# Kernel tuning notes

Hardware: AMD Instinct MI355X
Metric: run time of the kernel (lower is better)

Reference implementation:

```python
import jax, jax.numpy as jnp
import numpy as np

HEADS = 8
DIM_HEAD = 64
EPS = 1e-5

def setup_inputs() -> dict:
    key = jax.random.key(0)
    ks = jax.random.split(key, 5)
    c, inner = 320, HEADS * DIM_HEAD
    s = 0.02
    return {
        "hidden_states": jax.random.normal(ks[0], (4, c, 16, 32, 32), jnp.float32),
        "ln_w": jnp.ones((c,), jnp.float32),
        "ln_b": jnp.zeros((c,), jnp.float32),
        "Wq": jax.random.normal(ks[1], (inner, c), jnp.float32) * s,
        "Wk": jax.random.normal(ks[2], (inner, c), jnp.float32) * s,
        "Wv": jax.random.normal(ks[3], (inner, c), jnp.float32) * s,
        "Wo": jax.random.normal(ks[4], (c, inner), jnp.float32) * s,
        "bo": jnp.zeros((c,), jnp.float32),
    }

def reference(hidden_states, ln_w, ln_b, Wq, Wk, Wv, Wo, bo):
    b, c, t, h, w = hidden_states.shape
    scale = DIM_HEAD ** (-0.5)
    # (b h w) t c
    x0 = jnp.transpose(hidden_states, (0, 3, 4, 2, 1)).reshape(b * h * w, t, c)
    # LayerNorm over channel dim
    mu = jnp.mean(x0, axis=-1, keepdims=True)
    var = jnp.var(x0, axis=-1, keepdims=True)
    xn = (x0 - mu) / jnp.sqrt(var + EPS) * ln_w + ln_b
    # QKV projections (self-attention: encoder_hidden_states = normed hidden)
    q = xn @ Wq.T  # [B, t, inner]
    k = xn @ Wk.T
    v = xn @ Wv.T
    B = b * h * w
    q = q.reshape(B, t, HEADS, DIM_HEAD)
    k = k.reshape(B, t, HEADS, DIM_HEAD)
    v = v.reshape(B, t, HEADS, DIM_HEAD)
    scores = jnp.einsum("bqhd,bkhd->bhqk", q, k) * scale
    probs = jax.nn.softmax(scores, axis=-1)
    out = jnp.einsum("bhqk,bkhd->bqhd", probs, v).reshape(B, t, HEADS * DIM_HEAD)
    out = out @ Wo.T + bo
    out = out + x0  # residual (dropout p=0)
    # back to b c t h w
    return jnp.transpose(out.reshape(b, h, w, t, c), (0, 4, 3, 1, 2))
```

## Files before the change

kernel.cpp:

```cpp
#include <hip/hip_runtime.h>

#define TT 16
#define CC 320
#define NHEADS 8
#define DH 64
#define INNER 512

typedef float f32x4 __attribute__((ext_vector_type(4)));
typedef float f32x16 __attribute__((ext_vector_type(16)));
typedef short bf16x8 __attribute__((ext_vector_type(8)));
typedef unsigned short u16;

#define Z16 {0.f,0.f,0.f,0.f,0.f,0.f,0.f,0.f,0.f,0.f,0.f,0.f,0.f,0.f,0.f,0.f}

__device__ __forceinline__ float bf2f(u16 u){
    union { unsigned int i; float f; } v; v.i = ((unsigned int)u) << 16; return v.f;
}
__device__ __forceinline__ u16 f2bf(float f){
    union { float f; unsigned int i; } v; v.f = f;
    unsigned int x = v.i;
    return (u16)((x + 0x7fffu + ((x >> 16) & 1u)) >> 16);
}

__global__ __launch_bounds__(256) void k_wprep(const float* __restrict__ wq, const float* __restrict__ wk,
                                               const float* __restrict__ wv, const float* __restrict__ wo,
                                               u16* __restrict__ dqkv, u16* __restrict__ dwo){
    int blk = blockIdx.x;
    if (blk < 240){
        int gid  = blk * 256 + threadIdx.x;
        int lane = gid & 63;
        int f    = gid >> 6;
        int local = f % 12;
        int kl   = local & 1;
        int nblk = local >> 1;
        int c    = (f / 12) % 10;
        int hd   = f / 120;
        int kk   = c * 2 + kl;
        const float* W = (nblk < 2) ? wq : (nblk < 4) ? wk : wv;
        int n  = hd * DH + (nblk & 1) * 32 + (lane & 31);
        int k0 = kk * 16 + (lane >> 5) * 8;
        const float* src = W + (size_t)n * CC + k0;
        f32x4 v0 = *(const f32x4*)src;
        f32x4 v1 = *(const f32x4*)(src + 4);
        bf16x8 o;
        o[0] = (short)f2bf(v0[0]); o[1] = (short)f2bf(v0[1]);
        o[2] = (short)f2bf(v0[2]); o[3] = (short)f2bf(v0[3]);
        o[4] = (short)f2bf(v1[0]); o[5] = (short)f2bf(v1[1]);
        o[6] = (short)f2bf(v1[2]); o[7] = (short)f2bf(v1[3]);
        *(bf16x8*)(dqkv + (size_t)gid * 8) = o;
    } else {
        int gid  = (blk - 240) * 256 + threadIdx.x;
        int lane = gid & 63;
        int f    = gid >> 6;
        int kt   = f & 31;
        int nb   = f >> 5;
        int n  = nb * 32 + (lane & 31);
        int k0 = kt * 16 + (lane >> 5) * 8;
        const float* src = wo + (size_t)n * INNER + k0;
        f32x4 v0 = *(const f32x4*)src;
        f32x4 v1 = *(const f32x4*)(src + 4);
        bf16x8 o;
        o[0] = (short)f2bf(v0[0]); o[1] = (short)f2bf(v0[1]);
        o[2] = (short)f2bf(v0[2]); o[3] = (short)f2bf(v0[3]);
        o[4] = (short)f2bf(v1[0]); o[5] = (short)f2bf(v1[1]);
        o[6] = (short)f2bf(v1[2]); o[7] = (short)f2bf(v1[3]);
        *(bf16x8*)(dwo + (size_t)gid * 8) = o;
    }
}

__global__ __launch_bounds__(256) void k_ln(const float* __restrict__ x, const float* __restrict__ lnw,
                                            const float* __restrict__ lnb, u16* __restrict__ xnf){
    __shared__ float tile[CC][37];
    __shared__ float psum[32][36];
    __shared__ float psq[32][36];
    __shared__ float meanb[32];
    __shared__ float rstdb[32];
    __shared__ float lnw_s[CC];
    __shared__ float lnb_s[CC];

    int wg = blockIdx.x;
    int t = wg & 15, h = (wg >> 4) & 31, b = wg >> 9;
    int tid = threadIdx.x;
    const size_t base = ((size_t)(b * CC) * TT + t) * 1024 + h * 32;

    if (tid < CC - 256){ lnw_s[256 + tid] = lnw[256 + tid]; lnb_s[256 + tid] = lnb[256 + tid]; }
    lnw_s[tid] = lnw[tid]; lnb_s[tid] = lnb[tid];

    int w4 = (tid & 7) * 4, cg = tid >> 3;
    f32x4 s4 = {0.f,0.f,0.f,0.f}, q4 = {0.f,0.f,0.f,0.f};
    for (int i = 0; i < 10; ++i){
        int c = cg * 10 + i;
        f32x4 v = *(const f32x4*)(x + base + (size_t)c * 16384 + w4);
        tile[c][w4 + 0] = v[0]; tile[c][w4 + 1] = v[1];
        tile[c][w4 + 2] = v[2]; tile[c][w4 + 3] = v[3];
        s4 += v; q4 += v * v;
    }
    psum[cg][w4 + 0] = s4[0]; psum[cg][w4 + 1] = s4[1]; psum[cg][w4 + 2] = s4[2]; psum[cg][w4 + 3] = s4[3];
    psq [cg][w4 + 0] = q4[0]; psq [cg][w4 + 1] = q4[1]; psq [cg][w4 + 2] = q4[2]; psq [cg][w4 + 3] = q4[3];
    __syncthreads();

    if (tid < 32){
        float s = 0.f, q = 0.f;
        for (int g = 0; g < 32; ++g){ s += psum[g][tid]; q += psq[g][tid]; }
        float mean = s * (1.f / CC);
        float var  = q * (1.f / CC) - mean * mean;
        meanb[tid] = mean;
        rstdb[tid] = rsqrtf(var + 1e-5f);
    }
    __syncthreads();

    int s_base = (b * 32 + h) * 32;
    #pragma unroll
    for (int j = 0; j < 5; ++j){
        int u = tid + 256 * j;
        int w = u / 40, c8 = u % 40;
        float mean = meanb[w], rstd = rstdb[w];
        int s = s_base + w;
        int row = ((s & 1) << 4) | t;
        int kk = c8 >> 1;
        int lane_f = ((c8 & 1) << 5) | row;
        size_t m32 = (size_t)(s >> 1);
        bf16x8 o;
        #pragma unroll
        for (int e = 0; e < 8; ++e){
            int c = c8 * 8 + e;
            float nv = (tile[c][w] - mean) * rstd * lnw_s[c] + lnb_s[c];
            o[e] = (short)f2bf(nv);
        }
        *(bf16x8*)(xnf + ((size_t)(m32 * 20 + kk) * 64 + lane_f) * 8) = o;
    }
}

#define QH(w,s,r,c) smem[((((w)*2+(s))*16+(r))*72) + (c)]
#define KH(w,s,r,c) smem[9216 + ((((w)*2+(s))*16+(r))*72) + (c)]
#define VT(w,s,d,k) smem[18432 + ((((w)*2+(s))*64+(d))*36) + (k)]

__global__ __launch_bounds__(256, 2) void k_attn(const u16* __restrict__ xnf,
                                                 const u16* __restrict__ wqkv,
                                                 u16* __restrict__ aot){
    __shared__ u16 smem[36864];

    const int tid  = threadIdx.x;
    const int lane = tid & 63;
    const int wid  = tid >> 6;
    const int l31  = lane & 31;
    const int h32  = lane >> 5;
    const int l15  = lane & 15;
    const int g4   = lane >> 4;
    const int m32  = blockIdx.x * 4 + wid;
    const f32x4 zero4 = {0.f, 0.f, 0.f, 0.f};

    #pragma unroll
    for (int j = 0; j < 32; ++j){
        int idx = j * 64 + lane;
        int smp = idx >> 10;
        int d   = (idx >> 4) & 63;
        VT(wid, smp, d, 16 + (idx & 15)) = 0;
    }

    bf16x8 a_f[20];
    {
        const u16* xp = xnf + ((size_t)m32 * 20 * 64 + lane) * 8;
        #pragma unroll
        for (int kk = 0; kk < 20; ++kk)
            a_f[kk] = *(const bf16x8*)(xp + kk * 512);
    }

    #define STAGE(hd_, c_) do {                                                        \
        const u16* gsrc_ = wqkv + ((size_t)((hd_) * 10 + (c_)) * 6144);                \
        u16* ldst_ = (u16*)smem + ((c_) % 3) * 6144;                                   \
        _Pragma("unroll")                                                              \
        for (int i_ = 0; i_ < 3; ++i_)                                                 \
            __builtin_amdgcn_global_load_lds(                                          \
                (const __attribute__((address_space(1))) void*)(gsrc_ + (tid + i_ * 256) * 8), \
                (__attribute__((address_space(3))) void*)(ldst_ + (tid + i_ * 256) * 8),       \
                16, 0, 0);                                                             \
    } while (0)

    for (int hd = 0; hd < NHEADS; ++hd){
        __builtin_amdgcn_sched_barrier(0);
        __builtin_amdgcn_s_barrier();
        __builtin_amdgcn_sched_barrier(0);

        STAGE(hd, 0);

        f32x16 acc[6];
        #pragma unroll
        for (int nb = 0; nb < 6; ++nb) acc[nb] = (f32x16)Z16;

        #pragma unroll
        for (int c = 0; c < 10; ++c){
            asm volatile("s_waitcnt vmcnt(0)" ::: "memory");
            __builtin_amdgcn_sched_barrier(0);
            __builtin_amdgcn_s_barrier();
            __builtin_amdgcn_sched_barrier(0);
            if (c < 9) STAGE(hd, c + 1);
            const u16* wb = (const u16*)smem + (c % 3) * 6144;
            #pragma unroll
            for (int kl = 0; kl < 2; ++kl){
                #pragma unroll
                for (int nb = 0; nb < 6; ++nb){
                    bf16x8 b = *(const bf16x8*)(wb + (nb * 2 + kl) * 512 + lane * 8);
                    acc[nb] = __builtin_amdgcn_mfma_f32_32x32x16_bf16(a_f[c * 2 + kl], b, acc[nb], 0, 0, 0);
                }
            }
            __builtin_amdgcn_sched_barrier(0);
        }
        __builtin_amdgcn_s_barrier();
        __builtin_amdgcn_sched_barrier(0);

        #pragma unroll
        for (int r = 0; r < 16; ++r){
            int row = (r & 3) + 8 * (r >> 2) + 4 * h32;
            int smp = row >> 4, tr = row & 15;
            QH(wid, smp, tr, l31)      = f2bf(acc[0][r] * 0.125f);
            QH(wid, smp, tr, 32 + l31) = f2bf(acc[1][r] * 0.125f);
            KH(wid, smp, tr, l31)      = f2bf(acc[2][r]);
            KH(wid, smp, tr, 32 + l31) = f2bf(acc[3][r]);
            VT(wid, smp, l31, tr)      = f2bf(acc[4][r]);
            VT(wid, smp, 32 + l31, tr) = f2bf(acc[5][r]);
        }

        #pragma unroll
        for (int smp = 0; smp < 2; ++smp){
            f32x4 sc = zero4;
            #pragma unroll
            for (int k0 = 0; k0 < DH; k0 += 32){
                bf16x8 qa = *(const bf16x8*)&QH(wid, smp, l15, k0 + g4 * 8);
                bf16x8 kb = *(const bf16x8*)&KH(wid, smp, l15, k0 + g4 * 8);
                sc = __builtin_amdgcn_mfma_f32_16x16x32_bf16(qa, kb, sc, 0, 0, 0);
            }
            f32x4 pr;
            #pragma unroll
            for (int r = 0; r < 4; ++r){
                float m = sc[r];
                m = fmaxf(m, __shfl_xor(m, 1)); m = fmaxf(m, __shfl_xor(m, 2));
                m = fmaxf(m, __shfl_xor(m, 4)); m = fmaxf(m, __shfl_xor(m, 8));
                float e = __expf(sc[r] - m);
                float ss = e;
                ss += __shfl_xor(ss, 1); ss += __shfl_xor(ss, 2);
                ss += __shfl_xor(ss, 4); ss += __shfl_xor(ss, 8);
                pr[r] = e / ss;
            }
            #pragma unroll
            for (int r = 0; r < 4; ++r){
                QH(wid, smp, g4 * 4 + r, l15) = f2bf(pr[r]);
                QH(wid, smp, g4 * 4 + r, 16 + l15) = 0;
            }
            bf16x8 pa = *(const bf16x8*)&QH(wid, smp, l15, g4 * 8);
            #pragma unroll
            for (int nb = 0; nb < 4; ++nb){
                bf16x8 vb = *(const bf16x8*)&VT(wid, smp, nb * 16 + l15, g4 * 8);
                f32x4 at = __builtin_amdgcn_mfma_f32_16x16x32_bf16(pa, vb, zero4, 0, 0, 0);
                #pragma unroll
                for (int r = 0; r < 4; ++r)
                    KH(wid, smp, g4 * 4 + r, nb * 16 + l15) = f2bf(at[r]);
            }
            const size_t sg = (size_t)m32 * 2 + smp;
            #pragma unroll
            for (int kkl = 0; kkl < 2; ++kkl){
                bf16x8 o8 = *(const bf16x8*)&KH(wid, smp, l15, kkl * 32 + g4 * 8);
                *(bf16x8*)(aot + ((size_t)l15 * 4096 + sg) * 512 + hd * 64 + kkl * 32 + g4 * 8) = o8;
            }
        }
    }
    #undef STAGE
}

__global__ __launch_bounds__(256) void k_oproj_res(const u16* __restrict__ aot, const u16* __restrict__ wof,
                                                   const float* __restrict__ bo, const float* __restrict__ x,
                                                   float* __restrict__ out){
    __shared__ u16 atile[32 * 516];
    __shared__ float otile[4][32 * 36];

    const int tid  = threadIdx.x;
    const int lane = tid & 63;
    const int wid  = tid >> 6;
    const int l31  = lane & 31;
    const int h32  = lane >> 5;
    int wg = blockIdx.x;
    int t = wg & 15, h = (wg >> 4) & 31, b = wg >> 9;
    const int s0 = (b * 32 + h) * 32;

    {
        const u16* src = aot + ((size_t)t * 4096 + s0) * 512;
        #pragma unroll
        for (int i = 0; i < 8; ++i){
            int flat = tid + 256 * i;
            int row = flat >> 6, c16 = flat & 63;
            bf16x8 v = *(const bf16x8*)(src + (size_t)flat * 8);
            *(bf16x8*)(atile + row * 516 + c16 * 8) = v;
        }
    }
    __syncthreads();

    const int nb_start = (wid < 2) ? wid * 3 : 6 + (wid - 2) * 2;
    const int nb_count = (wid < 2) ? 3 : 2;

    for (int j = 0; j < nb_count; ++j){
        const int nb = nb_start + j;
        f32x16 acc = (f32x16)Z16;
        const u16* wp = wof + ((size_t)(nb * 32) * 64 + lane) * 8;
        #pragma unroll
        for (int kt = 0; kt < 32; ++kt){
            bf16x8 af = *(const bf16x8*)(atile + l31 * 516 + kt * 16 + h32 * 8);
            bf16x8 bf = *(const bf16x8*)(wp + (size_t)kt * 512);
            acc = __builtin_amdgcn_mfma_f32_32x32x16_bf16(af, bf, acc, 0, 0, 0);
        }
        float bias_v = bo[nb * 32 + l31];
        #pragma unroll
        for (int r = 0; r < 16; ++r){
            int row = (r & 3) + 8 * (r >> 2) + 4 * h32;
            otile[wid][l31 * 36 + row] = acc[r] + bias_v;
        }
        int cl = lane >> 3;
        int w4 = (lane & 7) * 4;
        #pragma unroll
        for (int ci = 0; ci < 4; ++ci){
            int c = ci * 8 + cl;
            size_t idx = ((size_t)(b * CC + nb * 32 + c) * TT + t) * 1024 + h * 32 + w4;
            f32x4 ov = *(const f32x4*)(&otile[wid][c * 36 + w4]);
            f32x4 xv = *(const f32x4*)(x + idx);
            *(f32x4*)(out + idx) = xv + ov;
        }
    }
}

extern "C" void kernel_launch(void* const* d_in, const int* in_sizes, int n_in,
                              void* d_out, int out_size, void* d_ws, size_t ws_size,
                              hipStream_t stream){
    const float* hid = (const float*)d_in[0];
    const float* lnw = (const float*)d_in[1];
    const float* lnb = (const float*)d_in[2];
    const float* Wq  = (const float*)d_in[3];
    const float* Wk  = (const float*)d_in[4];
    const float* Wv  = (const float*)d_in[5];
    const float* Wo  = (const float*)d_in[6];
    const float* bo  = (const float*)d_in[7];

    char* ws = (char*)d_ws;
    u16* wqkv = (u16*)ws;
    u16* wo_f = wqkv + (size_t)960 * 512;
    u16* aot  = wo_f + 163840;
    u16* xn   = aot + (size_t)TT * 4096 * INNER;

    k_wprep    <<<320, 256, 0, stream>>>(Wq, Wk, Wv, Wo, wqkv, wo_f);
    k_ln       <<<2048, 256, 0, stream>>>(hid, lnw, lnb, xn);
    k_attn     <<<512, 256, 0, stream>>>(xn, wqkv, aot);
    k_oproj_res<<<2048, 256, 0, stream>>>(aot, wo_f, bo, hid, (float*)d_out);
}
```

Before: 210.3 us.

## Merge weight prep with LayerNorm and widen attention blocks to eight waves

The weight-conversion and LayerNorm kernels become one launch that dispatches on block index, which removes one launch and the gap between kernels. The attention kernel now runs 512-thread blocks of eight waves over twice the LDS. Each staged QKV weight chunk (four k-steps, double-buffered) is shared by twice as many waves, which halves weight re-streaming per output row. The trade-offs are an extra barrier per chunk and an LDS footprint that likely allows only one block per CU.

```diff
diff --git a/kernel.cpp b/kernel.cpp
--- a/kernel.cpp
+++ b/kernel.cpp
@@ -22,20 +22,32 @@
     return (u16)((x + 0x7fffu + ((x >> 16) & 1u)) >> 16);
 }
 
-__global__ __launch_bounds__(256) void k_wprep(const float* __restrict__ wq, const float* __restrict__ wk,
-                                               const float* __restrict__ wv, const float* __restrict__ wo,
-                                               u16* __restrict__ dqkv, u16* __restrict__ dwo){
+__global__ __launch_bounds__(256) void k_prep(const float* __restrict__ wq, const float* __restrict__ wk,
+                                              const float* __restrict__ wv, const float* __restrict__ wo,
+                                              const float* __restrict__ lnw, const float* __restrict__ lnb,
+                                              const float* __restrict__ x,
+                                              u16* __restrict__ dqkv, u16* __restrict__ dwo,
+                                              u16* __restrict__ xnf){
+    __shared__ float tile[CC][37];
+    __shared__ float psum[32][36];
+    __shared__ float psq[32][36];
+    __shared__ float meanb[32];
+    __shared__ float rstdb[32];
+    __shared__ float lnw_s[CC];
+    __shared__ float lnb_s[CC];
+
     int blk = blockIdx.x;
+    int tid = threadIdx.x;
+
     if (blk < 240){
-        int gid  = blk * 256 + threadIdx.x;
+        int gid  = blk * 256 + tid;
         int lane = gid & 63;
         int f    = gid >> 6;
-        int local = f % 12;
-        int kl   = local & 1;
-        int nblk = local >> 1;
-        int c    = (f / 12) % 10;
+        int kl   = f & 3;
+        int nblk = (f >> 2) % 6;
+        int c    = ((f >> 2) / 6) % 5;
         int hd   = f / 120;
-        int kk   = c * 2 + kl;
+        int kk   = c * 4 + kl;
         const float* W = (nblk < 2) ? wq : (nblk < 4) ? wk : wv;
         int n  = hd * DH + (nblk & 1) * 32 + (lane & 31);
         int k0 = kk * 16 + (lane >> 5) * 8;
@@ -48,8 +60,10 @@
         o[4] = (short)f2bf(v1[0]); o[5] = (short)f2bf(v1[1]);
         o[6] = (short)f2bf(v1[2]); o[7] = (short)f2bf(v1[3]);
         *(bf16x8*)(dqkv + (size_t)gid * 8) = o;
-    } else {
-        int gid  = (blk - 240) * 256 + threadIdx.x;
+        return;
+    }
+    if (blk < 320){
+        int gid  = (blk - 240) * 256 + tid;
         int lane = gid & 63;
         int f    = gid >> 6;
         int kt   = f & 31;
@@ -65,22 +79,11 @@
         o[4] = (short)f2bf(v1[0]); o[5] = (short)f2bf(v1[1]);
         o[6] = (short)f2bf(v1[2]); o[7] = (short)f2bf(v1[3]);
         *(bf16x8*)(dwo + (size_t)gid * 8) = o;
-    }
-}
-
-__global__ __launch_bounds__(256) void k_ln(const float* __restrict__ x, const float* __restrict__ lnw,
-                                            const float* __restrict__ lnb, u16* __restrict__ xnf){
-    __shared__ float tile[CC][37];
-    __shared__ float psum[32][36];
-    __shared__ float psq[32][36];
-    __shared__ float meanb[32];
-    __shared__ float rstdb[32];
-    __shared__ float lnw_s[CC];
-    __shared__ float lnb_s[CC];
-
-    int wg = blockIdx.x;
+        return;
+    }
+
+    int wg = blk - 320;
     int t = wg & 15, h = (wg >> 4) & 31, b = wg >> 9;
-    int tid = threadIdx.x;
     const size_t base = ((size_t)(b * CC) * TT + t) * 1024 + h * 32;
 
     if (tid < CC - 256){ lnw_s[256 + tid] = lnw[256 + tid]; lnb_s[256 + tid] = lnb[256 + tid]; }
@@ -132,13 +135,13 @@
 }
 
 #define QH(w,s,r,c) smem[((((w)*2+(s))*16+(r))*72) + (c)]
-#define KH(w,s,r,c) smem[9216 + ((((w)*2+(s))*16+(r))*72) + (c)]
-#define VT(w,s,d,k) smem[18432 + ((((w)*2+(s))*64+(d))*36) + (k)]
-
-__global__ __launch_bounds__(256, 2) void k_attn(const u16* __restrict__ xnf,
+#define KH(w,s,r,c) smem[18432 + ((((w)*2+(s))*16+(r))*72) + (c)]
+#define VT(w,s,d,k) smem[36864 + ((((w)*2+(s))*64+(d))*36) + (k)]
+
+__global__ __launch_bounds__(512, 2) void k_attn(const u16* __restrict__ xnf,
                                                  const u16* __restrict__ wqkv,
                                                  u16* __restrict__ aot){
-    __shared__ u16 smem[36864];
+    __shared__ u16 smem[73728];
 
     const int tid  = threadIdx.x;
     const int lane = tid & 63;
@@ -147,7 +150,7 @@
     const int h32  = lane >> 5;
     const int l15  = lane & 15;
     const int g4   = lane >> 4;
-    const int m32  = blockIdx.x * 4 + wid;
+    const int m32  = blockIdx.x * 8 + wid;
     const f32x4 zero4 = {0.f, 0.f, 0.f, 0.f};
 
     #pragma unroll
@@ -167,13 +170,13 @@
     }
 
     #define STAGE(hd_, c_) do {                                                        \
-        const u16* gsrc_ = wqkv + ((size_t)((hd_) * 10 + (c_)) * 6144);                \
-        u16* ldst_ = (u16*)smem + ((c_) % 3) * 6144;                                   \
+        const u16* gsrc_ = wqkv + ((size_t)((hd_) * 5 + (c_)) * 12288);                \
+        u16* ldst_ = (u16*)smem + ((c_) & 1) * 12288;                                  \
         _Pragma("unroll")                                                              \
         for (int i_ = 0; i_ < 3; ++i_)                                                 \
             __builtin_amdgcn_global_load_lds(                                          \
-                (const __attribute__((address_space(1))) void*)(gsrc_ + (tid + i_ * 256) * 8), \
-                (__attribute__((address_space(3))) void*)(ldst_ + (tid + i_ * 256) * 8),       \
+                (const __attribute__((address_space(1))) void*)(gsrc_ + (tid + i_ * 512) * 8), \
+                (__attribute__((address_space(3))) void*)(ldst_ + (tid + i_ * 512) * 8),       \
                 16, 0, 0);                                                             \
     } while (0)
 
@@ -189,25 +192,25 @@
         for (int nb = 0; nb < 6; ++nb) acc[nb] = (f32x16)Z16;
 
         #pragma unroll
-        for (int c = 0; c < 10; ++c){
+        for (int c = 0; c < 5; ++c){
             asm volatile("s_waitcnt vmcnt(0)" ::: "memory");
             __builtin_amdgcn_sched_barrier(0);
             __builtin_amdgcn_s_barrier();
             __builtin_amdgcn_sched_barrier(0);
-            if (c < 9) STAGE(hd, c + 1);
-            const u16* wb = (const u16*)smem + (c % 3) * 6144;
-            #pragma unroll
-            for (int kl = 0; kl < 2; ++kl){
+            if (c < 4) STAGE(hd, c + 1);
+            const u16* wb = (const u16*)smem + (c & 1) * 12288;
+            #pragma unroll
+            for (int kl = 0; kl < 4; ++kl){
                 #pragma unroll
                 for (int nb = 0; nb < 6; ++nb){
-                    bf16x8 b = *(const bf16x8*)(wb + (nb * 2 + kl) * 512 + lane * 8);
-                    acc[nb] = __builtin_amdgcn_mfma_f32_32x32x16_bf16(a_f[c * 2 + kl], b, acc[nb], 0, 0, 0);
+                    bf16x8 b = *(const bf16x8*)(wb + (nb * 4 + kl) * 512 + lane * 8);
+                    acc[nb] = __builtin_amdgcn_mfma_f32_32x32x16_bf16(a_f[c * 4 + kl], b, acc[nb], 0, 0, 0);
                 }
             }
             __builtin_amdgcn_sched_barrier(0);
-        }
-        __builtin_amdgcn_s_barrier();
-        __builtin_amdgcn_sched_barrier(0);
+            __builtin_amdgcn_s_barrier();
+            __builtin_amdgcn_sched_barrier(0);
+        }
 
         #pragma unroll
         for (int r = 0; r < 16; ++r){
@@ -344,8 +347,7 @@
     u16* aot  = wo_f + 163840;
     u16* xn   = aot + (size_t)TT * 4096 * INNER;
 
-    k_wprep    <<<320, 256, 0, stream>>>(Wq, Wk, Wv, Wo, wqkv, wo_f);
-    k_ln       <<<2048, 256, 0, stream>>>(hid, lnw, lnb, xn);
-    k_attn     <<<512, 256, 0, stream>>>(xn, wqkv, aot);
+    k_prep     <<<2368, 256, 0, stream>>>(Wq, Wk, Wv, Wo, lnw, lnb, hid, wqkv, wo_f, xn);
+    k_attn     <<<256, 512, 0, stream>>>(xn, wqkv, aot);
     k_oproj_res<<<2048, 256, 0, stream>>>(aot, wo_f, bo, hid, (float*)d_out);
 }
```

Measured after the change: 200.0 us. 1.05x faster.
